# Optimization experiments

Measured on AMD Instinct MI355X. Metric: run time of the kernel, lower is better.

## Reference

```python
import jax, jax.numpy as jnp
import numpy as np

B, N, DIM, H = 1, 512, 384, 8
SK, SV, PK, PV = 16, 16, 4, 4
PAIR = 128
EPS = 1e-8


def _rand_rotations(key, b, n):
    m = jax.random.normal(key, (b, n, 3, 3), dtype=jnp.float32)
    q, _ = jnp.linalg.qr(m)  # orthonormal frames
    return q


def setup_inputs() -> dict:
    key = jax.random.key(0)
    ks = jax.random.split(key, 16)
    w = lambda k, shape: jax.random.normal(k, shape, dtype=jnp.float32) * 0.02
    inp = {
        "x": jax.random.normal(ks[0], (B, N, DIM), dtype=jnp.float32),
        "pairwise_repr": jax.random.normal(ks[1], (B, N, N, PAIR), dtype=jnp.float32),
        "rotations": _rand_rotations(ks[2], B, N),
        "translations": jax.random.normal(ks[3], (B, N, 3), dtype=jnp.float32),
        "W_sq": w(ks[4], (DIM, H * SK)),
        "W_sk": w(ks[5], (DIM, H * SK)),
        "W_sv": w(ks[6], (DIM, H * SV)),
        "W_pq": w(ks[7], (DIM, H * PK * 3)),
        "W_pk": w(ks[8], (DIM, H * PK * 3)),
        "W_pv": w(ks[9], (DIM, H * PV * 3)),
        "W_pair": w(ks[10], (PAIR, H)),
        "b_pair": jnp.zeros((H,), dtype=jnp.float32),
        # softplus(point_weights) == 1 at init, per the original log(e-1) init
        "point_weights": jnp.full((H,), float(np.log(np.e - 1.0)), dtype=jnp.float32),
        "W_out": w(ks[11], (H * (SV + PV * 3 + PV + PAIR), DIM)),
        "b_out": jnp.zeros((DIM,), dtype=jnp.float32),
    }
    return inp


def reference(x, pairwise_repr, rotations, translations,
              W_sq, W_sk, W_sv, W_pq, W_pk, W_pv,
              W_pair, b_pair, point_weights, W_out, b_out):
    b, n, _ = x.shape
    scalar_scale = (3 * SK) ** -0.5          # 3 logit terms
    point_scale = ((3 * PK) * (9.0 / 2.0)) ** -0.5
    pair_scale = 3.0 ** -0.5

    q_s = (x @ W_sq).reshape(b, n, H, SK)
    k_s = (x @ W_sk).reshape(b, n, H, SK)
    v_s = (x @ W_sv).reshape(b, n, H, SV)

    def to_global_points(W, d):
        p = (x @ W).reshape(b, n, H, d, 3)           # local-frame points
        p = jnp.einsum('bnhdc,bncr->bnhdr', p, rotations)
        return p + translations[:, :, None, None, :]  # global frame

    q_p = to_global_points(W_pq, PK)
    k_p = to_global_points(W_pk, PK)
    v_p = to_global_points(W_pv, PV)

    # scalar attention logits
    logits = jnp.einsum('bihd,bjhd->bhij', q_s, k_s) * scalar_scale
    # pairwise bias logits
    pair_bias = jnp.einsum('bijp,ph->bhij', pairwise_repr, W_pair) + b_pair[None, :, None, None]
    logits = logits + pair_bias * pair_scale
    # point-distance logits
    diff = q_p[:, :, None] - k_p[:, None]            # (b, i, j, h, d, 3)
    dist2 = jnp.sum(diff * diff, axis=(-1, -2))      # (b, i, j, h)
    pw = jax.nn.softplus(point_weights)              # (h,)
    logits = logits - 0.5 * point_scale * jnp.transpose(dist2, (0, 3, 1, 2)) * pw[None, :, None, None]

    attn = jax.nn.softmax(logits, axis=-1)           # (b, h, i, j)

    out_s = jnp.einsum('bhij,bjhd->bihd', attn, v_s).reshape(b, n, H * SV)
    out_pair = jnp.einsum('bhij,bijp->bihp', attn, pairwise_repr).reshape(b, n, H * PAIR)
    pts = jnp.einsum('bhij,bjhdc->bihdc', attn, v_p)  # global-frame value points
    # rotate back to local frame with R^T
    pts_local = jnp.einsum('bihdc,bicr->bihdr',
                           pts - translations[:, :, None, None, :],
                           jnp.swapaxes(rotations, -1, -2))
    pts_norm = jnp.sqrt(jnp.sum(pts_local ** 2, axis=-1) + EPS)

    feats = jnp.concatenate([
        out_s,
        pts_local.reshape(b, n, H * PV * 3),
        pts_norm.reshape(b, n, H * PV),
        out_pair,
    ], axis=-1)
    return feats @ W_out + b_out
```

## Files before the change

### kernel.cpp

```cpp
#include <hip/hip_runtime.h>
#include <hip/hip_bf16.h>
#include <math.h>

#define NN 512
#define DIMX 384
#define HH 8
#define PAIRD 128

#define SCALAR_SCALE 0.144337567297406f
#define POINT_SCALE  0.136082763487954f
#define PAIR_SCALE   0.577350269189626f

#define KSL 8
#define KPER 160
#define PCH 1264

__global__ __launch_bounds__(256) void k_proj_gemm(
    const float* __restrict__ x,
    const float* __restrict__ Wsq, const float* __restrict__ Wsk, const float* __restrict__ Wsv,
    const float* __restrict__ Wpq, const float* __restrict__ Wpk, const float* __restrict__ Wpv,
    float* __restrict__ qs, float* __restrict__ ks, float* __restrict__ vs,
    float* __restrict__ plq, float* __restrict__ plk, float* __restrict__ plv)
{
    const int m0 = blockIdx.x * 64;
    const int t  = blockIdx.y;
    int ldw, c0;
    const float* W;
    float* out;
    if (t < 12) {
        const float* Ws[3] = {Wsq, Wsk, Wsv};
        float* outs[3] = {qs, ks, vs};
        W = Ws[t >> 2]; out = outs[t >> 2]; c0 = (t & 3) * 32; ldw = 128;
    } else {
        const int u = t - 12;
        const float* Wp[3] = {Wpq, Wpk, Wpv};
        float* outp[3] = {plq, plk, plv};
        W = Wp[u / 3]; out = outp[u / 3]; c0 = (u % 3) * 32; ldw = 96;
    }
    const int tid = threadIdx.x;
    __shared__ float xs[32][68];
    __shared__ float Bs[32][36];
    const int tx = tid & 15, ty = tid >> 4;
    float acc[4][2] = {};

    for (int kt = 0; kt < DIMX; kt += 32) {
        #pragma unroll
        for (int it = 0; it < 2; ++it) {
            int l = tid + it * 256;
            int row = l >> 3, kq = l & 7;
            float4 a = *(const float4*)&x[(size_t)(m0 + row) * DIMX + kt + kq * 4];
            xs[kq*4+0][row] = a.x; xs[kq*4+1][row] = a.y;
            xs[kq*4+2][row] = a.z; xs[kq*4+3][row] = a.w;
        }
        {
            int kk = tid >> 3, nq = tid & 7;
            float4 b = *(const float4*)&W[(size_t)(kt + kk) * ldw + c0 + nq * 4];
            *(float4*)&Bs[kk][nq * 4] = b;
        }
        __syncthreads();
        #pragma unroll
        for (int k = 0; k < 32; ++k) {
            float4 a  = *(const float4*)&xs[k][ty * 4];
            float2 bv = *(const float2*)&Bs[k][tx * 2];
            acc[0][0] += a.x * bv.x; acc[0][1] += a.x * bv.y;
            acc[1][0] += a.y * bv.x; acc[1][1] += a.y * bv.y;
            acc[2][0] += a.z * bv.x; acc[2][1] += a.z * bv.y;
            acc[3][0] += a.w * bv.x; acc[3][1] += a.w * bv.y;
        }
        __syncthreads();
    }
    #pragma unroll
    for (int r = 0; r < 4; ++r) {
        float2 v = make_float2(acc[r][0], acc[r][1]);
        *(float2*)&out[(size_t)(m0 + ty * 4 + r) * ldw + c0 + tx * 2] = v;
    }
}

__global__ __launch_bounds__(256) void k_frames(
    const float* __restrict__ plq, const float* __restrict__ plk, const float* __restrict__ plv,
    const float* __restrict__ rot, const float* __restrict__ trans,
    float* __restrict__ qp, float* __restrict__ kp, float* __restrict__ vp)
{
    int g = blockIdx.x * 256 + threadIdx.x;
    int m = g >> 14;
    int rem = g & 16383;
    int i = rem >> 5;
    int p = rem & 31;
    const float* pl = (m == 0 ? plq : (m == 1 ? plk : plv));
    float*       o  = (m == 0 ? qp  : (m == 1 ? kp  : vp));
    const float* l = &pl[(size_t)i * 96 + p * 3];
    const float* R = &rot[(size_t)i * 9];
    const float* T = &trans[(size_t)i * 3];
    float l0 = l[0], l1 = l[1], l2 = l[2];
    float* op = o + (size_t)i * 96 + p * 3;
    #pragma unroll
    for (int c = 0; c < 3; ++c)
        op[c] = l0 * R[0 * 3 + c] + l1 * R[1 * 3 + c] + l2 * R[2 * 3 + c] + T[c];
}

__global__ __launch_bounds__(256) void k_attn(
    const float* __restrict__ pair,
    const float* __restrict__ qs, const float* __restrict__ ks,
    const float* __restrict__ qp, const float* __restrict__ kp,
    const float* __restrict__ vs, const float* __restrict__ vp,
    const float* __restrict__ Wpair, const float* __restrict__ bpair,
    const float* __restrict__ pwts,
    float* __restrict__ attnp)
{
    const int jc  = blockIdx.x;
    const int i   = blockIdx.y;
    const int tid = threadIdx.x;

    __shared__ float smem[5768];
    float* pt   = smem;
    float* wpt  = smem + 4224;
    float* wt   = smem + 5248;
    float* cb   = smem + 5536;
    float* qs_s = smem + 5544;
    float* qp_s = smem + 5672;

    for (int l = tid; l < 1024; l += 256) {
        float v = Wpair[l];
        wpt[(l & 7) * 128 + (l >> 3)] = v;
    }
    if (tid < 32) ((float4*)qs_s)[tid] = ((const float4*)(qs + (size_t)i * 128))[tid];
    if (tid < 24) ((float4*)qp_s)[tid] = ((const float4*)(qp + (size_t)i * 96))[tid];

    const int g   = tid & 7;
    const int jjL = tid >> 3;
    const int h2  = tid >> 5;
    const int jj2 = tid & 31;
    const int jg  = h2, pq = jj2;

    const float bp_h = bpair[g];
    const float pw_h = log1pf(__expf(pwts[g]));

    float m_run = -1e30f, l_run = 0.f;
    float4 accP[8];
    #pragma unroll
    for (int z = 0; z < 8; ++z) accP[z] = make_float4(0, 0, 0, 0);
    float4 accS = make_float4(0, 0, 0, 0);
    float4 accV = make_float4(0, 0, 0, 0);

    const float4* pair4 = (const float4*)(pair + ((size_t)i * NN + jc * 128) * PAIRD);
    const float4* vs4   = (const float4*)vs;
    const float4* vp4   = (const float4*)vp;

    float4 r0 = pair4[tid], r1 = pair4[tid + 256], r2 = pair4[tid + 512], r3 = pair4[tid + 768];

    for (int t = 0; t < 4; ++t) {
        *(float4*)&pt[(tid >> 5) * 132 + (tid & 31) * 4]         = r0;
        *(float4*)&pt[((tid + 256) >> 5) * 132 + (tid & 31) * 4] = r1;
        *(float4*)&pt[((tid + 512) >> 5) * 132 + (tid & 31) * 4] = r2;
        *(float4*)&pt[((tid + 768) >> 5) * 132 + (tid & 31) * 4] = r3;
        __syncthreads();

        if (t < 3) {
            const float4* nx = pair4 + (size_t)(t + 1) * 1024;
            r0 = nx[tid]; r1 = nx[tid + 256]; r2 = nx[tid + 512]; r3 = nx[tid + 768];
        }

        float b[8] = {0,0,0,0,0,0,0,0};
        #pragma unroll
        for (int q = 0; q < 4; ++q) {
            float4 a = *(const float4*)&pt[jjL * 132 + q * 32 + g * 4];
            #pragma unroll
            for (int z = 0; z < 8; ++z) {
                float4 w = *(const float4*)&wpt[z * 128 + q * 32 + g * 4];
                b[z] += a.x * w.x + a.y * w.y + a.z * w.z + a.w * w.w;
            }
        }
        float v0, v1, v2, v3, w0, w1, bias;
        {
            float o0 = __shfl_xor(b[0], 4), o1 = __shfl_xor(b[1], 4);
            float o2 = __shfl_xor(b[2], 4), o3 = __shfl_xor(b[3], 4);
            float o4 = __shfl_xor(b[4], 4), o5 = __shfl_xor(b[5], 4);
            float o6 = __shfl_xor(b[6], 4), o7 = __shfl_xor(b[7], 4);
            bool s2 = (g & 4);
            v0 = s2 ? (b[4] + o4) : (b[0] + o0);
            v1 = s2 ? (b[5] + o5) : (b[1] + o1);
            v2 = s2 ? (b[6] + o6) : (b[2] + o2);
            v3 = s2 ? (b[7] + o7) : (b[3] + o3);
            float p0 = __shfl_xor(v0, 2), p1 = __shfl_xor(v1, 2);
            float p2 = __shfl_xor(v2, 2), p3 = __shfl_xor(v3, 2);
            bool s1 = (g & 2);
            w0 = s1 ? (v2 + p2) : (v0 + p0);
            w1 = s1 ? (v3 + p3) : (v1 + p1);
            float q0 = __shfl_xor(w0, 1), q1 = __shfl_xor(w1, 1);
            bias = (g & 1) ? (w1 + q1) : (w0 + q0);
        }

        const int j = jc * 128 + t * 32 + jjL;
        float sc = 0.f;
        {
            const float4* kr4 = (const float4*)(ks + (size_t)j * 128 + g * 16);
            const float4* qr4 = (const float4*)&qs_s[g * 16];
            #pragma unroll
            for (int q = 0; q < 4; ++q) {
                float4 kq = kr4[q], qq = qr4[q];
                sc += qq.x * kq.x + qq.y * kq.y + qq.z * kq.z + qq.w * kq.w;
            }
        }
        float d2 = 0.f;
        {
            const float4* kp4 = (const float4*)(kp + (size_t)j * 96 + g * 12);
            const float4* qp4 = (const float4*)&qp_s[g * 12];
            #pragma unroll
            for (int q = 0; q < 3; ++q) {
                float4 kq = kp4[q], qq = qp4[q];
                float dx = qq.x - kq.x, dy = qq.y - kq.y, dz = qq.z - kq.z, dw = qq.w - kq.w;
                d2 += dx * dx + dy * dy + dz * dz + dw * dw;
            }
        }
        wt[g * 36 + jjL] = sc * SCALAR_SCALE + (bias + bp_h) * PAIR_SCALE
                         - 0.5f * POINT_SCALE * pw_h * d2;
        __syncthreads();

        {
            float lg = wt[h2 * 36 + jj2];
            float tm = lg;
            #pragma unroll
            for (int off = 16; off > 0; off >>= 1) tm = fmaxf(tm, __shfl_xor(tm, off));
            float m_new = fmaxf(m_run, tm);
            float corr  = __expf(m_run - m_new);
            float p     = __expf(lg - m_new);
            float ps    = p;
            #pragma unroll
            for (int off = 16; off > 0; off >>= 1) ps += __shfl_xor(ps, off);
            l_run = l_run * corr + ps;
            m_run = m_new;
            wt[h2 * 36 + jj2] = p;
            if (jj2 == 0) cb[h2] = corr;
        }
        __syncthreads();

        #pragma unroll
        for (int z = 0; z < 8; ++z) {
            float c = cb[z];
            accP[z].x *= c; accP[z].y *= c; accP[z].z *= c; accP[z].w *= c;
        }
        {
            float c = cb[pq >> 2];
            accS.x *= c; accS.y *= c; accS.z *= c; accS.w *= c;
        }
        if (pq < 24) {
            float c = cb[pq / 3];
            accV.x *= c; accV.y *= c; accV.z *= c; accV.w *= c;
        }
        #pragma unroll
        for (int jo = 0; jo < 4; ++jo) {
            const int jl = jo * 8 + jg;
            const int jglob = jc * 128 + t * 32 + jl;
            float4 pr = *(const float4*)&pt[jl * 132 + pq * 4];
            #pragma unroll
            for (int z = 0; z < 8; ++z) {
                float a = wt[z * 36 + jl];
                accP[z].x += a * pr.x; accP[z].y += a * pr.y;
                accP[z].z += a * pr.z; accP[z].w += a * pr.w;
            }
            {
                float a = wt[(pq >> 2) * 36 + jl];
                float4 v = vs4[(size_t)jglob * 32 + pq];
                accS.x += a * v.x; accS.y += a * v.y; accS.z += a * v.z; accS.w += a * v.w;
            }
            if (pq < 24) {
                float a = wt[(pq / 3) * 36 + jl];
                float4 v = vp4[(size_t)jglob * 24 + pq];
                accV.x += a * v.x; accV.y += a * v.y; accV.z += a * v.z; accV.w += a * v.w;
            }
        }
        __syncthreads();
    }

    float* attnc = attnp + ((size_t)i * 4 + jc) * PCH;
    if (jj2 == 0) { attnc[1248 + h2] = m_run; attnc[1256 + h2] = l_run; }

    #pragma unroll
    for (int z = 0; z < 8; ++z) {
        accP[z].x += __shfl_xor(accP[z].x, 32); accP[z].y += __shfl_xor(accP[z].y, 32);
        accP[z].z += __shfl_xor(accP[z].z, 32); accP[z].w += __shfl_xor(accP[z].w, 32);
    }
    accS.x += __shfl_xor(accS.x, 32); accS.y += __shfl_xor(accS.y, 32);
    accS.z += __shfl_xor(accS.z, 32); accS.w += __shfl_xor(accS.w, 32);
    accV.x += __shfl_xor(accV.x, 32); accV.y += __shfl_xor(accV.y, 32);
    accV.z += __shfl_xor(accV.z, 32); accV.w += __shfl_xor(accV.w, 32);

    float4* redP = (float4*)smem;
    float4* redS = (float4*)(smem + 4224);
    float4* redV = (float4*)(smem + 4736);
    const int jgp = jg >> 1;
    if ((jg & 1) == 0) {
        #pragma unroll
        for (int z = 0; z < 8; ++z) redP[(jgp * 8 + z) * 32 + pq] = accP[z];
        redS[jgp * 32 + pq] = accS;
        if (pq < 24) redV[jgp * 24 + pq] = accV;
    }
    __syncthreads();

    {
        const int z = tid >> 5, p4 = tid & 31;
        float4 s = redP[z * 32 + p4];
        #pragma unroll
        for (int gg = 1; gg < 4; ++gg) {
            float4 v = redP[(gg * 8 + z) * 32 + p4];
            s.x += v.x; s.y += v.y; s.z += v.z; s.w += v.w;
        }
        *(float4*)&attnc[z * 128 + p4 * 4] = s;
    }
    if (tid < 32) {
        float4 s = redS[tid];
        #pragma unroll
        for (int gg = 1; gg < 4; ++gg) {
            float4 v = redS[gg * 32 + tid];
            s.x += v.x; s.y += v.y; s.z += v.z; s.w += v.w;
        }
        *(float4*)&attnc[1024 + tid * 4] = s;
    } else if (tid < 56) {
        const int pc = tid - 32;
        float4 s = redV[pc];
        #pragma unroll
        for (int gg = 1; gg < 4; ++gg) {
            float4 v = redV[gg * 24 + pc];
            s.x += v.x; s.y += v.y; s.z += v.z; s.w += v.w;
        }
        *(float4*)&attnc[1152 + pc * 4] = s;
    }
}

__global__ __launch_bounds__(256) void k_attn_merge(
    const float* __restrict__ attnp,
    const float* __restrict__ rot, const float* __restrict__ trans,
    float* __restrict__ feats)
{
    const int i = blockIdx.x;
    const int tid = threadIdx.x;
    __shared__ float sm_m[32], sm_l[32], sW[32], sL[8], pts_s[96];

    const float* base = attnp + (size_t)i * 4 * PCH;
    if (tid < 32) {
        int jcx = tid >> 3, h = tid & 7;
        sm_m[jcx * 8 + h] = base[jcx * PCH + 1248 + h];
        sm_l[jcx * 8 + h] = base[jcx * PCH + 1256 + h];
    }
    __syncthreads();
    if (tid < 8) {
        const int h = tid;
        float M = fmaxf(fmaxf(sm_m[h], sm_m[8 + h]), fmaxf(sm_m[16 + h], sm_m[24 + h]));
        float L = 0.f;
        #pragma unroll
        for (int jcx = 0; jcx < 4; ++jcx) {
            float w = __expf(sm_m[jcx * 8 + h] - M);
            L += sm_l[jcx * 8 + h] * w;
            sW[jcx * 8 + h] = w;
        }
        sL[h] = L;
    }
    __syncthreads();

    {
        const int h = tid >> 5, pq = tid & 31;
        float4 s = make_float4(0, 0, 0, 0);
        #pragma unroll
        for (int jcx = 0; jcx < 4; ++jcx) {
            float4 a = *(const float4*)&base[jcx * PCH + h * 128 + pq * 4];
            float w = sW[jcx * 8 + h];
            s.x += a.x * w; s.y += a.y * w; s.z += a.z * w; s.w += a.w * w;
        }
        float inv = 1.f / sL[h];
        s.x *= inv; s.y *= inv; s.z *= inv; s.w *= inv;
        ((float4*)&feats[(size_t)i * 1280 + 256])[tid] = s;
    }
    if (tid < 32) {
        const int h = tid >> 2;
        float4 s = make_float4(0, 0, 0, 0);
        #pragma unroll
        for (int jcx = 0; jcx < 4; ++jcx) {
            float4 a = *(const float4*)&base[jcx * PCH + 1024 + tid * 4];
            float w = sW[jcx * 8 + h];
            s.x += a.x * w; s.y += a.y * w; s.z += a.z * w; s.w += a.w * w;
        }
        float inv = 1.f / sL[h];
        s.x *= inv; s.y *= inv; s.z *= inv; s.w *= inv;
        ((float4*)&feats[(size_t)i * 1280])[tid] = s;
    } else if (tid < 56) {
        const int pc = tid - 32;
        const int h = pc / 3;
        float4 s = make_float4(0, 0, 0, 0);
        #pragma unroll
        for (int jcx = 0; jcx < 4; ++jcx) {
            float4 a = *(const float4*)&base[jcx * PCH + 1152 + pc * 4];
            float w = sW[jcx * 8 + h];
            s.x += a.x * w; s.y += a.y * w; s.z += a.z * w; s.w += a.w * w;
        }
        float inv = 1.f / sL[h];
        s.x *= inv; s.y *= inv; s.z *= inv; s.w *= inv;
        ((float4*)pts_s)[pc] = s;
    }
    __syncthreads();

    if (tid < 32) {
        const float* R = &rot[(size_t)i * 9];
        const float* T = &trans[(size_t)i * 3];
        float px = pts_s[tid * 3 + 0] - T[0];
        float py = pts_s[tid * 3 + 1] - T[1];
        float pz = pts_s[tid * 3 + 2] - T[2];
        float n2 = 0.f;
        float* fo = feats + (size_t)i * 1280;
        #pragma unroll
        for (int r = 0; r < 3; ++r) {
            float lr = px * R[r * 3 + 0] + py * R[r * 3 + 1] + pz * R[r * 3 + 2];
            fo[128 + tid * 3 + r] = lr;
            n2 += lr * lr;
        }
        fo[224 + tid] = sqrtf(n2 + 1e-8f);
    }
}

__global__ __launch_bounds__(256) void k_final_gemm(
    const float* __restrict__ feats, const float* __restrict__ Wout,
    float* __restrict__ partial)
{
    const int m0 = blockIdx.x * 128;
    const int n0 = blockIdx.y * 128;
    const int ks = blockIdx.z;
    const int tid = threadIdx.x;
    const int k0 = ks * KPER;
    __shared__ float As[16][132];
    __shared__ float Bs[16][132];
    const int tx = tid & 15, ty = tid >> 4;
    float acc[8][8] = {};

    for (int kt = 0; kt < KPER; kt += 16) {
        #pragma unroll
        for (int it = 0; it < 2; ++it) {
            const int l = tid + it * 256;
            const int row = l >> 2, kq = l & 3;
            float4 a = *(const float4*)&feats[(size_t)(m0 + row) * 1280 + k0 + kt + kq * 4];
            As[kq * 4 + 0][row] = a.x; As[kq * 4 + 1][row] = a.y;
            As[kq * 4 + 2][row] = a.z; As[kq * 4 + 3][row] = a.w;
            const int kk = l >> 5, nq = l & 31;
            float4 b = *(const float4*)&Wout[(size_t)(k0 + kt + kk) * 384 + n0 + nq * 4];
            *(float4*)&Bs[kk][nq * 4] = b;
        }
        __syncthreads();
        #pragma unroll
        for (int k = 0; k < 16; ++k) {
            float4 a0 = *(const float4*)&As[k][ty * 8];
            float4 a1 = *(const float4*)&As[k][ty * 8 + 4];
            float4 b0 = *(const float4*)&Bs[k][tx * 8];
            float4 b1 = *(const float4*)&Bs[k][tx * 8 + 4];
            float am[8] = {a0.x, a0.y, a0.z, a0.w, a1.x, a1.y, a1.z, a1.w};
            float bn[8] = {b0.x, b0.y, b0.z, b0.w, b1.x, b1.y, b1.z, b1.w};
            #pragma unroll
            for (int r = 0; r < 8; ++r)
                #pragma unroll
                for (int c = 0; c < 8; ++c)
                    acc[r][c] += am[r] * bn[c];
        }
        __syncthreads();
    }
    float* po = partial + (size_t)ks * (512 * 384);
    #pragma unroll
    for (int r = 0; r < 8; ++r) {
        *(float4*)&po[(size_t)(m0 + ty * 8 + r) * 384 + n0 + tx * 8]     = *(float4*)&acc[r][0];
        *(float4*)&po[(size_t)(m0 + ty * 8 + r) * 384 + n0 + tx * 8 + 4] = *(float4*)&acc[r][4];
    }
}

__global__ __launch_bounds__(256) void k_reduce(
    const float* __restrict__ partial, const float* __restrict__ bout,
    float* __restrict__ out)
{
    const int f = blockIdx.x * 256 + threadIdx.x;
    const int e = f * 4;
    const int col = e % 384;
    float4 acc = *(const float4*)&bout[col];
    #pragma unroll
    for (int s = 0; s < KSL; ++s) {
        float4 p = *(const float4*)&partial[(size_t)s * (512 * 384) + e];
        acc.x += p.x; acc.y += p.y; acc.z += p.z; acc.w += p.w;
    }
    *(float4*)&out[e] = acc;
}

extern "C" void kernel_launch(void* const* d_in, const int* in_sizes, int n_in,
                              void* d_out, int out_size, void* d_ws, size_t ws_size,
                              hipStream_t stream) {
    const float* x     = (const float*)d_in[0];
    const float* pair  = (const float*)d_in[1];
    const float* rot   = (const float*)d_in[2];
    const float* trans = (const float*)d_in[3];
    const float* Wsq   = (const float*)d_in[4];
    const float* Wsk   = (const float*)d_in[5];
    const float* Wsv   = (const float*)d_in[6];
    const float* Wpq   = (const float*)d_in[7];
    const float* Wpk   = (const float*)d_in[8];
    const float* Wpv   = (const float*)d_in[9];
    const float* Wpair = (const float*)d_in[10];
    const float* bpair = (const float*)d_in[11];
    const float* pwts  = (const float*)d_in[12];
    const float* Wout  = (const float*)d_in[13];
    const float* bout  = (const float*)d_in[14];

    float* ws      = (float*)d_ws;
    float* qs      = ws;
    float* ks      = qs + 512 * 128;
    float* vs      = ks + 512 * 128;
    float* qp      = vs + 512 * 128;
    float* kp      = qp + 512 * 96;
    float* vp      = kp + 512 * 96;
    float* feats   = vp + 512 * 96;
    float* attnp   = feats + 512 * 1280;
    float* partial = attnp;
    float* plq     = attnp + 2048 * PCH;
    float* plk     = plq + 512 * 96;
    float* plv     = plk + 512 * 96;

    k_proj_gemm<<<dim3(8, 21), 256, 0, stream>>>(x, Wsq, Wsk, Wsv, Wpq, Wpk, Wpv,
                                                 qs, ks, vs, plq, plk, plv);
    k_frames<<<192, 256, 0, stream>>>(plq, plk, plv, rot, trans, qp, kp, vp);
    k_attn<<<dim3(4, 512), 256, 0, stream>>>(pair, qs, ks, qp, kp, vs, vp,
                                             Wpair, bpair, pwts, attnp);
    k_attn_merge<<<512, 256, 0, stream>>>(attnp, rot, trans, feats);
    k_final_gemm<<<dim3(4, 3, KSL), 256, 0, stream>>>(feats, Wout, partial);
    k_reduce<<<192, 256, 0, stream>>>(partial, bout, (float*)d_out);
}
```

Measured before the change: 126.3 us.

## Precompute pair bias in a separate kernel and store it in bf16

Adds a k_bias kernel that projects pairwise_repr through W_pair into a per-(i,j,h) bias buffer stored as bf16. k_attn then reads that bias instead of computing it from a shared-memory pair tile. It loads pair values for the weighted sum directly from global memory, and double-buffers the softmax weight and correction arrays to drop one barrier per step. The intent is to shorten the attention kernel's per-step critical path and free shared memory. In exchange the 128 MB pairwise tensor is streamed twice, a bias buffer is written and re-read, and the bias loses precision to bf16.

```diff
diff --git a/kernel.cpp b/kernel.cpp
--- a/kernel.cpp
+++ b/kernel.cpp
@@ -14,6 +14,60 @@
 #define KSL 8
 #define KPER 160
 #define PCH 1264
+
+__global__ __launch_bounds__(256) void k_bias(
+    const float* __restrict__ pair, const float* __restrict__ Wpair,
+    __hip_bfloat16* __restrict__ bias)
+{
+    const int jc = blockIdx.x & 3;
+    const int i  = blockIdx.x >> 2;
+    const int tid = threadIdx.x;
+    const int b  = tid >> 5;
+    const int pq = tid & 31;
+
+    float wv[32];
+    {
+        const float4* W4 = (const float4*)(Wpair + pq * 32);
+        #pragma unroll
+        for (int q = 0; q < 8; ++q) {
+            float4 w = W4[q];
+            wv[q * 4 + 0] = w.x; wv[q * 4 + 1] = w.y;
+            wv[q * 4 + 2] = w.z; wv[q * 4 + 3] = w.w;
+        }
+    }
+    #pragma unroll
+    for (int it = 0; it < 4; ++it) {
+        const int j0 = jc * 128 + it * 32;
+        float cur[32];
+        #pragma unroll
+        for (int r = 0; r < 4; ++r) {
+            const int j = j0 + b + r * 8;
+            float4 a = *(const float4*)&pair[((size_t)i * NN + j) * PAIRD + pq * 4];
+            float ac[4] = {a.x, a.y, a.z, a.w};
+            #pragma unroll
+            for (int h = 0; h < 8; ++h) {
+                float s = 0.f;
+                #pragma unroll
+                for (int p = 0; p < 4; ++p) s += ac[p] * wv[p * 8 + h];
+                cur[r * 8 + h] = s;
+            }
+        }
+        #pragma unroll
+        for (int s5 = 0; s5 < 5; ++s5) {
+            const int m = 16 >> s5;
+            const bool up = (pq & m) != 0;
+            #pragma unroll
+            for (int u = 0; u < (16 >> s5); ++u) {
+                float lo = cur[u], hi = cur[u + (16 >> s5)];
+                float send = up ? lo : hi;
+                float got  = __shfl_xor(send, m);
+                cur[u] = up ? (hi + got) : (lo + got);
+            }
+        }
+        const int j = j0 + b + (pq >> 3) * 8;
+        bias[((size_t)i * NN + j) * 8 + (pq & 7)] = __float2bfloat16(cur[0]);
+    }
+}
 
 __global__ __launch_bounds__(256) void k_proj_gemm(
     const float* __restrict__ x,
@@ -103,28 +157,23 @@
     const float* __restrict__ qs, const float* __restrict__ ks,
     const float* __restrict__ qp, const float* __restrict__ kp,
     const float* __restrict__ vs, const float* __restrict__ vp,
-    const float* __restrict__ Wpair, const float* __restrict__ bpair,
-    const float* __restrict__ pwts,
+    const __hip_bfloat16* __restrict__ bias,
+    const float* __restrict__ bpair, const float* __restrict__ pwts,
     float* __restrict__ attnp)
 {
     const int jc  = blockIdx.x;
     const int i   = blockIdx.y;
     const int tid = threadIdx.x;
 
-    __shared__ float smem[5768];
-    float* pt   = smem;
-    float* wpt  = smem + 4224;
-    float* wt   = smem + 5248;
-    float* cb   = smem + 5536;
-    float* qs_s = smem + 5544;
-    float* qp_s = smem + 5672;
-
-    for (int l = tid; l < 1024; l += 256) {
-        float v = Wpair[l];
-        wpt[(l & 7) * 128 + (l >> 3)] = v;
-    }
+    __shared__ float smem[5120];
+    float* wtb  = smem;
+    float* cbb  = smem + 576;
+    float* qs_s = smem + 592;
+    float* qp_s = smem + 720;
+
     if (tid < 32) ((float4*)qs_s)[tid] = ((const float4*)(qs + (size_t)i * 128))[tid];
     if (tid < 24) ((float4*)qp_s)[tid] = ((const float4*)(qp + (size_t)i * 96))[tid];
+    __syncthreads();
 
     const int g   = tid & 7;
     const int jjL = tid >> 3;
@@ -142,57 +191,18 @@
     float4 accS = make_float4(0, 0, 0, 0);
     float4 accV = make_float4(0, 0, 0, 0);
 
-    const float4* pair4 = (const float4*)(pair + ((size_t)i * NN + jc * 128) * PAIRD);
+    const float4* pair4 = (const float4*)pair;
     const float4* vs4   = (const float4*)vs;
     const float4* vp4   = (const float4*)vp;
 
-    float4 r0 = pair4[tid], r1 = pair4[tid + 256], r2 = pair4[tid + 512], r3 = pair4[tid + 768];
-
     for (int t = 0; t < 4; ++t) {
-        *(float4*)&pt[(tid >> 5) * 132 + (tid & 31) * 4]         = r0;
-        *(float4*)&pt[((tid + 256) >> 5) * 132 + (tid & 31) * 4] = r1;
-        *(float4*)&pt[((tid + 512) >> 5) * 132 + (tid & 31) * 4] = r2;
-        *(float4*)&pt[((tid + 768) >> 5) * 132 + (tid & 31) * 4] = r3;
-        __syncthreads();
-
-        if (t < 3) {
-            const float4* nx = pair4 + (size_t)(t + 1) * 1024;
-            r0 = nx[tid]; r1 = nx[tid + 256]; r2 = nx[tid + 512]; r3 = nx[tid + 768];
-        }
-
-        float b[8] = {0,0,0,0,0,0,0,0};
-        #pragma unroll
-        for (int q = 0; q < 4; ++q) {
-            float4 a = *(const float4*)&pt[jjL * 132 + q * 32 + g * 4];
-            #pragma unroll
-            for (int z = 0; z < 8; ++z) {
-                float4 w = *(const float4*)&wpt[z * 128 + q * 32 + g * 4];
-                b[z] += a.x * w.x + a.y * w.y + a.z * w.z + a.w * w.w;
-            }
-        }
-        float v0, v1, v2, v3, w0, w1, bias;
+        float* wt = wtb + (t & 1) * 288;
+        float* cb = cbb + (t & 1) * 8;
+
         {
-            float o0 = __shfl_xor(b[0], 4), o1 = __shfl_xor(b[1], 4);
-            float o2 = __shfl_xor(b[2], 4), o3 = __shfl_xor(b[3], 4);
-            float o4 = __shfl_xor(b[4], 4), o5 = __shfl_xor(b[5], 4);
-            float o6 = __shfl_xor(b[6], 4), o7 = __shfl_xor(b[7], 4);
-            bool s2 = (g & 4);
-            v0 = s2 ? (b[4] + o4) : (b[0] + o0);
-            v1 = s2 ? (b[5] + o5) : (b[1] + o1);
-            v2 = s2 ? (b[6] + o6) : (b[2] + o2);
-            v3 = s2 ? (b[7] + o7) : (b[3] + o3);
-            float p0 = __shfl_xor(v0, 2), p1 = __shfl_xor(v1, 2);
-            float p2 = __shfl_xor(v2, 2), p3 = __shfl_xor(v3, 2);
-            bool s1 = (g & 2);
-            w0 = s1 ? (v2 + p2) : (v0 + p0);
-            w1 = s1 ? (v3 + p3) : (v1 + p1);
-            float q0 = __shfl_xor(w0, 1), q1 = __shfl_xor(w1, 1);
-            bias = (g & 1) ? (w1 + q1) : (w0 + q0);
-        }
-
-        const int j = jc * 128 + t * 32 + jjL;
-        float sc = 0.f;
-        {
+            const int j = jc * 128 + t * 32 + jjL;
+            float bv = __bfloat162float(bias[((size_t)i * NN + j) * 8 + g]);
+            float sc = 0.f;
             const float4* kr4 = (const float4*)(ks + (size_t)j * 128 + g * 16);
             const float4* qr4 = (const float4*)&qs_s[g * 16];
             #pragma unroll
@@ -200,9 +210,7 @@
                 float4 kq = kr4[q], qq = qr4[q];
                 sc += qq.x * kq.x + qq.y * kq.y + qq.z * kq.z + qq.w * kq.w;
             }
-        }
-        float d2 = 0.f;
-        {
+            float d2 = 0.f;
             const float4* kp4 = (const float4*)(kp + (size_t)j * 96 + g * 12);
             const float4* qp4 = (const float4*)&qp_s[g * 12];
             #pragma unroll
@@ -211,9 +219,9 @@
                 float dx = qq.x - kq.x, dy = qq.y - kq.y, dz = qq.z - kq.z, dw = qq.w - kq.w;
                 d2 += dx * dx + dy * dy + dz * dz + dw * dw;
             }
-        }
-        wt[g * 36 + jjL] = sc * SCALAR_SCALE + (bias + bp_h) * PAIR_SCALE
-                         - 0.5f * POINT_SCALE * pw_h * d2;
+            wt[g * 36 + jjL] = sc * SCALAR_SCALE + (bv + bp_h) * PAIR_SCALE
+                             - 0.5f * POINT_SCALE * pw_h * d2;
+        }
         __syncthreads();
 
         {
@@ -251,7 +259,7 @@
         for (int jo = 0; jo < 4; ++jo) {
             const int jl = jo * 8 + jg;
             const int jglob = jc * 128 + t * 32 + jl;
-            float4 pr = *(const float4*)&pt[jl * 132 + pq * 4];
+            float4 pr = pair4[((size_t)i * NN + jglob) * 32 + pq];
             #pragma unroll
             for (int z = 0; z < 8; ++z) {
                 float a = wt[z * 36 + jl];
@@ -269,8 +277,8 @@
                 accV.x += a * v.x; accV.y += a * v.y; accV.z += a * v.z; accV.w += a * v.w;
             }
         }
-        __syncthreads();
-    }
+    }
+    __syncthreads();
 
     float* attnc = attnp + ((size_t)i * 4 + jc) * PCH;
     if (jj2 == 0) { attnc[1248 + h2] = m_run; attnc[1256 + h2] = l_run; }
@@ -502,25 +510,28 @@
     const float* Wout  = (const float*)d_in[13];
     const float* bout  = (const float*)d_in[14];
 
-    float* ws      = (float*)d_ws;
-    float* qs      = ws;
-    float* ks      = qs + 512 * 128;
-    float* vs      = ks + 512 * 128;
-    float* qp      = vs + 512 * 128;
-    float* kp      = qp + 512 * 96;
-    float* vp      = kp + 512 * 96;
-    float* feats   = vp + 512 * 96;
-    float* attnp   = feats + 512 * 1280;
-    float* partial = attnp;
-    float* plq     = attnp + 2048 * PCH;
-    float* plk     = plq + 512 * 96;
-    float* plv     = plk + 512 * 96;
-
+    float* ws    = (float*)d_ws;
+    float* qs    = ws;
+    float* ks    = qs + 512 * 128;
+    float* vs    = ks + 512 * 128;
+    float* qp    = vs + 512 * 128;
+    float* kp    = qp + 512 * 96;
+    float* vp    = kp + 512 * 96;
+    float* feats = vp + 512 * 96;
+    float* biasF = feats + 512 * 1280;
+    float* attnp = biasF + 1048576;
+    float* plq   = attnp + 2048 * PCH;
+    float* plk   = plq + 512 * 96;
+    float* plv   = plk + 512 * 96;
+    __hip_bfloat16* bias = (__hip_bfloat16*)biasF;
+    float* partial = biasF;
+
+    k_bias<<<2048, 256, 0, stream>>>(pair, Wpair, bias);
     k_proj_gemm<<<dim3(8, 21), 256, 0, stream>>>(x, Wsq, Wsk, Wsv, Wpq, Wpk, Wpv,
                                                  qs, ks, vs, plq, plk, plv);
     k_frames<<<192, 256, 0, stream>>>(plq, plk, plv, rot, trans, qp, kp, vp);
     k_attn<<<dim3(4, 512), 256, 0, stream>>>(pair, qs, ks, qp, kp, vs, vp,
-                                             Wpair, bpair, pwts, attnp);
+                                             bias, bpair, pwts, attnp);
     k_attn_merge<<<512, 256, 0, stream>>>(attnp, rot, trans, feats);
     k_final_gemm<<<dim3(4, 3, KSL), 256, 0, stream>>>(feats, Wout, partial);
     k_reduce<<<192, 256, 0, stream>>>(partial, bout, (float*)d_out);
```

Result: slower. 134.2 us (+6.2%).
